# Kernel optimization log

Hardware: AMD Instinct MI355X
Metric: run time of the kernel (lower is better)

The kernel has to match this reference:

```python
import jax, jax.numpy as jnp
import numpy as np

B, S, D, HD, P = 4, 8192, 1024, 128, 32
EPS_LN = 1e-5

def setup_inputs() -> dict:
    key = jax.random.key(0)
    ks = jax.random.split(key, 12)
    x      = jax.random.normal(ks[0], (B, S, D), dtype=jnp.float32)
    W_proj = jax.random.normal(ks[1], (8, D, HD), dtype=jnp.float32) * 0.02
    freqs  = jax.random.normal(ks[2], (8, HD), dtype=jnp.float32) * 0.01
    W_pol  = jax.random.normal(ks[3], (8, HD, P), dtype=jnp.float32) * 0.05
    b_pol  = jnp.zeros((8, P), jnp.float32)
    W_imp1 = jax.random.normal(ks[4], (1, 16), dtype=jnp.float32) * 0.5
    b_imp1 = jnp.zeros((16,), jnp.float32)
    W_imp2 = jax.random.normal(ks[5], (16, 1), dtype=jnp.float32) * 0.5
    b_imp2 = jnp.zeros((1,), jnp.float32)
    W_out  = jax.random.normal(ks[6], (D, D), dtype=jnp.float32) * 0.02
    b_out  = jnp.zeros((D,), jnp.float32)
    gamma  = jnp.ones((D,), jnp.float32)
    beta   = jnp.zeros((D,), jnp.float32)
    return dict(x=x, W_proj=W_proj, freqs=freqs, W_pol=W_pol, b_pol=b_pol,
                W_imp1=W_imp1, b_imp1=b_imp1, W_imp2=W_imp2, b_imp2=b_imp2,
                W_out=W_out, b_out=b_out, gamma=gamma, beta=beta)

def reference(x, W_proj, freqs, W_pol, b_pol, W_imp1, b_imp1, W_imp2, b_imp2,
              W_out, b_out, gamma, beta):
    # heads[i] = (x @ W_proj[i]) * cos(pi * freqs[i])   -> (8, B, S, HD)
    heads = jnp.einsum('bsd,hde->hbse', x, W_proj) * jnp.cos(freqs * jnp.pi)[:, None, None, :]

    # --- GuaXiangDuiChong: impedance matrix (B, 8, 8) ---
    hm = heads.mean(axis=2)                                   # (8, B, HD)
    pv = jnp.tanh(jnp.einsum('hbd,hdp->bhp', hm, W_pol) + b_pol[None])  # (B, 8, P)
    pm = pv / jnp.maximum(jnp.linalg.norm(pv, axis=-1, keepdims=True), 1e-12)
    dp = jnp.einsum('bhp,bgp->bhg', pm, pm)                   # (B, 8, 8)
    z = jax.nn.gelu(dp[..., None] * W_imp1[0] + b_imp1, approximate=False)  # (B,8,8,16)
    imp = jax.nn.softplus(jnp.einsum('bhgk,ko->bhgo', z, W_imp2)[..., 0] + b_imp2[0])
    imp = imp * (1.0 - jnp.eye(8, dtype=imp.dtype))           # zero diagonal

    # --- head mixing. Causal masked-mean collapses to row scale (s+1)/S ---
    coeff = (0.1 / (1.0 + imp)) * (1.0 - jnp.eye(8, dtype=imp.dtype))  # (B,8,8), j!=i
    mix = jnp.einsum('big,gbsd->ibsd', coeff, heads)          # (8, B, S, HD)
    causal_scale = (jnp.arange(S, dtype=x.dtype) + 1.0) / S   # (S,)
    out_heads = heads + causal_scale[None, None, :, None] * mix

    merged = out_heads.transpose(1, 2, 0, 3).reshape(B, S, D)
    proj = jnp.einsum('bsd,de->bse', merged, W_out) + b_out   # dropout = identity (eval)
    y = proj + x
    mu = y.mean(axis=-1, keepdims=True)
    var = y.var(axis=-1, keepdims=True)
    y = (y - mu) * jax.lax.rsqrt(var + EPS_LN) * gamma + beta
    return y, imp
```

## Files before the change

kernel.cpp:

```cpp
#include <hip/hip_runtime.h>
#include <hip/hip_bf16.h>
#include <math.h>

typedef __bf16 bf16;
typedef __bf16 bf16x2 __attribute__((ext_vector_type(2)));
typedef __bf16 bf16x4 __attribute__((ext_vector_type(4)));
typedef __bf16 bf16x8 __attribute__((ext_vector_type(8)));
typedef float  f32x4  __attribute__((ext_vector_type(4)));

#define NB 4
#define SS 8192
#define DD 1024
#define MM 32768
#define KK 1024
#define NN 1024
#define PI_F 3.14159265358979323846f

__device__ __forceinline__ void gl2lds16(const bf16* g, bf16* l) {
    __builtin_amdgcn_global_load_lds(
        (const __attribute__((address_space(1))) void*)g,
        (__attribute__((address_space(3))) void*)l, 16, 0, 0);
}

__global__ __launch_bounds__(256) void prep_all(const float* __restrict__ x,
                                                bf16* __restrict__ xb,
                                                const float* __restrict__ W_proj,
                                                const float* __restrict__ freqs,
                                                const float* __restrict__ W_out,
                                                bf16* __restrict__ WbT1,
                                                bf16* __restrict__ WoT,
                                                float* __restrict__ hm) {
    int blk = blockIdx.x;
    if (blk < MM / 2) {
        size_t i = (size_t)blk * 2048 + threadIdx.x * 8;
        float4 v0 = *(const float4*)&x[i];
        float4 v1 = *(const float4*)&x[i + 4];
        bf16x8 o;
        o[0] = (bf16)v0.x; o[1] = (bf16)v0.y; o[2] = (bf16)v0.z; o[3] = (bf16)v0.w;
        o[4] = (bf16)v1.x; o[5] = (bf16)v1.y; o[6] = (bf16)v1.z; o[7] = (bf16)v1.w;
        *(bf16x8*)&xb[i] = o;
    } else {
        int idx = (blk - MM / 2) * 256 + threadIdx.x;
        int n = idx >> 10, k = idx & 1023;
        int h = n >> 7, d = n & 127;
        float c = cosf(PI_F * freqs[n]);
        WbT1[idx] = (bf16)(W_proj[(size_t)h * (DD * 128) + (size_t)k * 128 + d] * c);
        WoT[idx]  = (bf16)(W_out[(size_t)k * DD + n]);
        if (idx < NB * DD) hm[idx] = 0.0f;
    }
}


#define FENCE  asm volatile("" ::: "memory")
#define BARRIER do { FENCE; __builtin_amdgcn_s_barrier(); FENCE; } while (0)
#define PRIO1  __builtin_amdgcn_s_setprio(1)
#define PRIO0  __builtin_amdgcn_s_setprio(0)
#define VMC(N) asm volatile("s_waitcnt vmcnt(" #N ")" ::: "memory")
#define NOPS   ((void)0)

#define STG(g0, g1, uk, ldsBase)                                  \
    gl2lds16((g0) + (uk), &sm[(ldsBase) + w * 512]);              \
    gl2lds16((g1) + (uk), &sm[(ldsBase) + 4096 + w * 512]);

#define READ_A2(MQ, ab)                                                          \
    _Pragma("unroll") for (int m_ = 0; m_ < 4; ++m_) {                           \
        a[m_ * 2 + 0] = *(const bf16x8*)&sm[(ab) + aoff0 + ((MQ)*64 + m_*16)*64];\
        a[m_ * 2 + 1] = *(const bf16x8*)&sm[(ab) + aoff1 + ((MQ)*64 + m_*16)*64];\
    }
#define READ_B2(NQ, bfr, bb)                                                     \
    _Pragma("unroll") for (int n_ = 0; n_ < 2; ++n_) {                           \
        bfr[n_ * 2 + 0] = *(const bf16x8*)&sm[(bb) + boff0 + ((NQ)*32 + n_*16)*64];\
        bfr[n_ * 2 + 1] = *(const bf16x8*)&sm[(bb) + boff1 + ((NQ)*32 + n_*16)*64];\
    }

#define MFMA_Q(MQ, NQ, bfr)                                                    \
    _Pragma("unroll") for (int m_ = 0; m_ < 4; ++m_)                           \
    _Pragma("unroll") for (int n_ = 0; n_ < 2; ++n_)                           \
    _Pragma("unroll") for (int ks_ = 0; ks_ < 2; ++ks_)                        \
        acc[(MQ) * 4 + m_][(NQ) * 2 + n_] =                                    \
            __builtin_amdgcn_mfma_f32_16x16x32_bf16(                           \
                a[m_ * 2 + ks_], bfr[n_ * 2 + ks_],                            \
                acc[(MQ) * 4 + m_][(NQ) * 2 + n_], 0, 0, 0);

#define ITER(uk1, STGB2a, STGB2b, STGA2a, STGA2b, STGB3a, STGB3b, VM2, VM4)    \
  {                        \
    BARRIER;                                                                   \
    STG(gA00, gA01, (uk1), 16384); STG(gA10, gA11, (uk1), 24576);              \
    PRIO1; READ_A2(0, 0); READ_B2(0, blo, 32768); READ_B2(1, bhi, 32768);      \
    MFMA_Q(0, 0, blo); MFMA_Q(0, 1, bhi); PRIO0;                               \
                          \
    BARRIER;                                                                   \
    STGB2a; STGB2b; VM2;                                                       \
    PRIO1; READ_A2(1, 0); MFMA_Q(1, 1, bhi); MFMA_Q(1, 0, blo); PRIO0;         \
                         \
    BARRIER;                                                                   \
    STGA2a; STGA2b;                                                            \
    PRIO1; READ_A2(0, 16384); READ_B2(0, blo, 49152); READ_B2(1, bhi, 49152);  \
    MFMA_Q(0, 0, blo); MFMA_Q(0, 1, bhi); PRIO0;                               \
                          \
    BARRIER;                                                                   \
    STGB3a; STGB3b; VM4;                                                       \
    PRIO1; READ_A2(1, 16384); MFMA_Q(1, 1, bhi); MFMA_Q(1, 0, blo); PRIO0;     \
  }

template <int MODE>
__global__ __launch_bounds__(512, 2)
void gemm256(const bf16* __restrict__ A, int lda, const bf16* __restrict__ Bt,
             bf16* __restrict__ Cstr, const bf16* __restrict__ residb,
             const float* __restrict__ bias, float* __restrict__ hm) {
    __shared__ bf16 sm[65536];
    const int tid = threadIdx.x;
    const int lane = tid & 63, w = tid >> 6;
    const int wr = w >> 2, wc = w & 3;
    const int l15 = lane & 15, l4 = lane >> 4;

    int wg = blockIdx.x;
    int swz = (wg & 7) * 64 + (wg >> 3);
    const int mt = swz >> 2, ntile = swz & 3;
    const int row0 = mt * 256, col0 = ntile * 256;

    const int aoff0 = (wr * 128 + l15) * 64 + ((l4 ^ (l15 & 7)) << 3);
    const int aoff1 = aoff0 ^ 32;
    const int boff0 = (wc * 64 + l15) * 64 + ((l4 ^ (l15 & 7)) << 3);
    const int boff1 = boff0 ^ 32;

    const int srow = tid >> 3;
    const int scb  = (tid & 7) ^ (srow & 7);
    const bf16* gA00 = A + (size_t)(row0 + srow) * lda + scb * 8;
    const bf16* gA01 = gA00 + (size_t)64 * lda;
    const bf16* gA10 = gA00 + (size_t)128 * lda;
    const bf16* gA11 = gA00 + (size_t)192 * lda;
    const bf16* gB00 = Bt + (size_t)(col0 + srow) * 1024 + scb * 8;
    const bf16* gB01 = gB00 + 64 * 1024;
    const bf16* gB10 = gB00 + 128 * 1024;
    const bf16* gB11 = gB00 + 192 * 1024;

    f32x4 acc[8][4] = {};
    bf16x8 a[8], blo[4], bhi[4];

    STG(gA00, gA01, 0,  0);     STG(gA10, gA11, 0,  8192);
    STG(gB00, gB01, 0,  32768); STG(gB10, gB11, 0,  40960);
    STG(gB00, gB01, 64, 49152); STG(gB10, gB11, 64, 57344);
    VMC(4);

#pragma unroll 1
    for (int i = 0; i < 7; ++i) {
        const int uk1 = (2 * i + 1) * 64;
        const int uk2 = (2 * i + 2) * 64;
        const int uk3 = (2 * i + 3) * 64;
        ITER(uk1,
             STG(gB00, gB01, uk2, 32768), STG(gB10, gB11, uk2, 40960),
             STG(gA00, gA01, uk2, 0),     STG(gA10, gA11, uk2, 8192),
             STG(gB00, gB01, uk3, 49152), STG(gB10, gB11, uk3, 57344),
             VMC(4), VMC(4));
    }
    ITER(960, NOPS, NOPS, NOPS, NOPS, NOPS, NOPS, VMC(0), NOPS);

    if (MODE == 0) {
        const int batch = row0 >> 13;
#pragma unroll
        for (int mg = 0; mg < 8; ++mg) {
            int rbase = row0 + wr * 128 + (mg >> 2) * 64 + (mg & 3) * 16 + l4 * 4;
#pragma unroll
            for (int j = 0; j < 4; ++j) {
                size_t row = rbase + j;
#pragma unroll
                for (int ng = 0; ng < 4; ++ng) {
                    int col = col0 + wc * 64 + ng * 16 + l15;
                    Cstr[row * 2048 + col] = (bf16)acc[mg][ng][j];
                }
            }
        }
#pragma unroll
        for (int ng = 0; ng < 4; ++ng) {
            float s = 0;
#pragma unroll
            for (int mg = 0; mg < 8; ++mg)
#pragma unroll
                for (int j = 0; j < 4; ++j) s += acc[mg][ng][j];
            int col = col0 + wc * 64 + ng * 16 + l15;
            atomicAdd(&hm[batch * DD + col], s);
        }
    } else {
        float bi[4];
#pragma unroll
        for (int ng = 0; ng < 4; ++ng) bi[ng] = bias[col0 + wc * 64 + ng * 16 + l15];
#pragma unroll
        for (int mg = 0; mg < 8; ++mg) {
            int rbase = row0 + wr * 128 + (mg >> 2) * 64 + (mg & 3) * 16 + l4 * 4;
#pragma unroll
            for (int j = 0; j < 4; ++j) {
                size_t row = rbase + j;
#pragma unroll
                for (int ng = 0; ng < 4; ++ng) {
                    int col = col0 + wc * 64 + ng * 16 + l15;
                    Cstr[row * 2048 + col] =
                        (bf16)(acc[mg][ng][j] + bi[ng] + (float)residb[row * 1024 + col]);
                }
            }
        }
    }
}

__global__ __launch_bounds__(1024) void imp_k(const float* __restrict__ hm,
                                              const float* __restrict__ W_pol,
                                              const float* __restrict__ b_pol,
                                              const float* __restrict__ W_imp1,
                                              const float* __restrict__ b_imp1,
                                              const float* __restrict__ W_imp2,
                                              const float* __restrict__ b_imp2,
                                              float* __restrict__ imp_out,
                                              float* __restrict__ coeff) {
    __shared__ float pm_s[32][32];
    int tid = threadIdx.x;
    int bh = tid >> 5, p = tid & 31;
    int b = bh >> 3, h = bh & 7;
    float a = b_pol[h * 32 + p];
    for (int d = 0; d < 128; ++d)
        a += hm[b * DD + h * 128 + d] * (1.0f / SS) * W_pol[(h * 128 + d) * 32 + p];
    float pv = tanhf(a);
    pm_s[bh][p] = pv;
    __syncthreads();
    float ss = 0;
    for (int q = 0; q < 32; ++q) ss += pm_s[bh][q] * pm_s[bh][q];
    float pmv = pv / fmaxf(sqrtf(ss), 1e-12f);
    __syncthreads();
    pm_s[bh][p] = pmv;
    __syncthreads();
    if (tid < 256) {
        int b2 = tid >> 6, h2 = (tid >> 3) & 7, g = tid & 7;
        float dp = 0;
        for (int q = 0; q < 32; ++q) dp += pm_s[b2 * 8 + h2][q] * pm_s[b2 * 8 + g][q];
        float a2 = 0;
        for (int kk = 0; kk < 16; ++kk) {
            float zin = dp * W_imp1[kk] + b_imp1[kk];
            float zg = 0.5f * zin * (1.0f + erff(zin * 0.70710678118654752f));
            a2 += zg * W_imp2[kk];
        }
        float spin = a2 + b_imp2[0];
        float impv = (spin > 20.0f) ? spin : log1pf(expf(spin));
        if (h2 == g) impv = 0.0f;
        imp_out[tid] = impv;
        coeff[tid] = (h2 == g) ? 0.0f : 0.1f / (1.0f + impv);
    }
}

__global__ __launch_bounds__(256) void mix_k(const char* __restrict__ slots,
                                             const float* __restrict__ coeff,
                                             char* __restrict__ slots_w) {
    __shared__ float cf[64];
    int tid = threadIdx.x;
    size_t r0 = (size_t)blockIdx.x * 16;
    int b = (int)(r0 >> 13);
    if (tid < 64) cf[tid] = coeff[b * 64 + tid];
    __syncthreads();
    size_t r = r0 + (tid >> 4);
    int dd = tid & 15;
    int s = (int)(r & (SS - 1));
    float cs = (float)(s + 1) * (1.0f / SS);
    const bf16* hrow = (const bf16*)(slots + r * 4096);
    bf16* mrow = (bf16*)(slots_w + r * 4096 + 2048);
    float v[8][8];
#pragma unroll
    for (int g = 0; g < 8; ++g) {
        bf16x8 t8 = *(const bf16x8*)&hrow[g * 128 + dd * 8];
#pragma unroll
        for (int e = 0; e < 8; ++e) v[g][e] = (float)t8[e];
    }
#pragma unroll
    for (int h = 0; h < 8; ++h) {
        bf16x8 o;
#pragma unroll
        for (int e = 0; e < 8; ++e) {
            float acc = 0;
#pragma unroll
            for (int g = 0; g < 8; ++g) acc += cf[h * 8 + g] * v[g][e];
            o[e] = (bf16)(v[h][e] + cs * acc);
        }
        *(bf16x8*)&mrow[h * 128 + dd * 8] = o;
    }
}

__global__ __launch_bounds__(256) void ln_k(char* __restrict__ slots,
                                            const float* __restrict__ gamma,
                                            const float* __restrict__ beta) {
    size_t r = blockIdx.x;
    int tid = threadIdx.x;
    const bf16* zrow = (const bf16*)(slots + r * 4096);
    float* yrow = (float*)(slots + r * 4096);
    int e0 = tid * 4;
    bf16x4 zv = *(const bf16x4*)&zrow[e0];
    float vx = (float)zv[0], vy = (float)zv[1], vz = (float)zv[2], vw = (float)zv[3];
    float sum = vx + vy + vz + vw;
    float sq  = vx * vx + vy * vy + vz * vz + vw * vw;
    for (int off = 32; off > 0; off >>= 1) {
        sum += __shfl_down(sum, off);
        sq  += __shfl_down(sq, off);
    }
    __shared__ float red[8];
    int lane = tid & 63, wv = tid >> 6;
    if (lane == 0) { red[wv] = sum; red[4 + wv] = sq; }
    __syncthreads();
    float tot = red[0] + red[1] + red[2] + red[3];
    float tsq = red[4] + red[5] + red[6] + red[7];
    float mu  = tot * (1.0f / DD);
    float var = tsq * (1.0f / DD) - mu * mu;
    float rs  = rsqrtf(var + 1e-5f);
    float4 g4 = *(const float4*)&gamma[e0];
    float4 b4 = *(const float4*)&beta[e0];
    float4 o;
    o.x = (vx - mu) * rs * g4.x + b4.x;
    o.y = (vy - mu) * rs * g4.y + b4.y;
    o.z = (vz - mu) * rs * g4.z + b4.z;
    o.w = (vw - mu) * rs * g4.w + b4.w;
    *(float4*)&yrow[e0] = o;
}

extern "C" void kernel_launch(void* const* d_in, const int* in_sizes, int n_in,
                              void* d_out, int out_size, void* d_ws, size_t ws_size,
                              hipStream_t stream) {
    const float* x      = (const float*)d_in[0];
    const float* W_proj = (const float*)d_in[1];
    const float* freqs  = (const float*)d_in[2];
    const float* W_pol  = (const float*)d_in[3];
    const float* b_pol  = (const float*)d_in[4];
    const float* W_imp1 = (const float*)d_in[5];
    const float* b_imp1 = (const float*)d_in[6];
    const float* W_imp2 = (const float*)d_in[7];
    const float* b_imp2 = (const float*)d_in[8];
    const float* W_out  = (const float*)d_in[9];
    const float* b_out  = (const float*)d_in[10];
    const float* gamma  = (const float*)d_in[11];
    const float* beta   = (const float*)d_in[12];

    char* ws = (char*)d_ws;
    bf16* xb     = (bf16*)ws;
    bf16* WbT1   = (bf16*)(ws + ((size_t)64 << 20));
    bf16* WoT    = (bf16*)(ws + ((size_t)66 << 20));
    float* hm    = (float*)(ws + ((size_t)68 << 20));
    float* coeff = (float*)(ws + ((size_t)68 << 20) + 16384);

    char* slots = (char*)d_out;
    float* imp_out = (float*)d_out + (size_t)MM * DD;

    prep_all<<<MM / 2 + 4096, 256, 0, stream>>>(x, xb, W_proj, freqs, W_out,
                                                WbT1, WoT, hm);

    gemm256<0><<<512, 512, 0, stream>>>(xb, 1024, WbT1, (bf16*)slots,
                                        nullptr, nullptr, hm);

    imp_k<<<1, 1024, 0, stream>>>(hm, W_pol, b_pol, W_imp1, b_imp1, W_imp2, b_imp2,
                                  imp_out, coeff);

    mix_k<<<MM / 16, 256, 0, stream>>>(slots, coeff, slots);

    gemm256<1><<<512, 512, 0, stream>>>((const bf16*)slots + 1024, 2048, WoT,
                                        (bf16*)slots, xb, b_out, nullptr);

    ln_k<<<MM, 256, 0, stream>>>(slots, gamma, beta);
}
```

Before: 272.3 us.

## Split GEMM main loop into finer barrier phases, parallelize impedance, batch LayerNorm rows

```diff
diff --git a/kernel.cpp b/kernel.cpp
--- a/kernel.cpp
+++ b/kernel.cpp
@@ -50,7 +50,6 @@
     }
 }
 
-
 #define FENCE  asm volatile("" ::: "memory")
 #define BARRIER do { FENCE; __builtin_amdgcn_s_barrier(); FENCE; } while (0)
 #define PRIO1  __builtin_amdgcn_s_setprio(1)
@@ -82,25 +81,23 @@
                 a[m_ * 2 + ks_], bfr[n_ * 2 + ks_],                            \
                 acc[(MQ) * 4 + m_][(NQ) * 2 + n_], 0, 0, 0);
 
-#define ITER(uk1, STGB2a, STGB2b, STGA2a, STGA2b, STGB3a, STGB3b, VM2, VM4)    \
-  {                        \
-    BARRIER;                                                                   \
-    STG(gA00, gA01, (uk1), 16384); STG(gA10, gA11, (uk1), 24576);              \
-    PRIO1; READ_A2(0, 0); READ_B2(0, blo, 32768); READ_B2(1, bhi, 32768);      \
-    MFMA_Q(0, 0, blo); MFMA_Q(0, 1, bhi); PRIO0;                               \
-                          \
-    BARRIER;                                                                   \
-    STGB2a; STGB2b; VM2;                                                       \
-    PRIO1; READ_A2(1, 0); MFMA_Q(1, 1, bhi); MFMA_Q(1, 0, blo); PRIO0;         \
-                         \
-    BARRIER;                                                                   \
-    STGA2a; STGA2b;                                                            \
-    PRIO1; READ_A2(0, 16384); READ_B2(0, blo, 49152); READ_B2(1, bhi, 49152);  \
-    MFMA_Q(0, 0, blo); MFMA_Q(0, 1, bhi); PRIO0;                               \
-                          \
-    BARRIER;                                                                   \
-    STGB3a; STGB3b; VM4;                                                       \
-    PRIO1; READ_A2(1, 16384); MFMA_Q(1, 1, bhi); MFMA_Q(1, 0, blo); PRIO0;     \
+#define ITER(uk1, STG3, STG4, STG5, STG6, STG7, STG8, VM4, VM8)                \
+  { BARRIER; STG(gA00, gA01, (uk1), 16384);                                    \
+    PRIO1; READ_A2(0, 0); READ_B2(0, blo, 32768); MFMA_Q(0, 0, blo); PRIO0;    \
+    BARRIER; STG(gA10, gA11, (uk1), 24576);                                    \
+    PRIO1; READ_B2(1, bhi, 32768); MFMA_Q(0, 1, bhi); PRIO0;                   \
+    BARRIER; STG3;                                                             \
+    PRIO1; READ_A2(1, 0); MFMA_Q(1, 1, bhi); PRIO0;                            \
+    BARRIER; STG4; VM4;                                                        \
+    PRIO1; MFMA_Q(1, 0, blo); PRIO0;                                           \
+    BARRIER; STG5;                                                             \
+    PRIO1; READ_A2(0, 16384); READ_B2(0, blo, 49152); MFMA_Q(0, 0, blo); PRIO0;\
+    BARRIER; STG6;                                                             \
+    PRIO1; READ_B2(1, bhi, 49152); MFMA_Q(0, 1, bhi); PRIO0;                   \
+    BARRIER; STG7;                                                             \
+    PRIO1; READ_A2(1, 16384); MFMA_Q(1, 1, bhi); PRIO0;                        \
+    BARRIER; STG8; VM8;                                                        \
+    PRIO1; MFMA_Q(1, 0, blo); PRIO0;                                           \
   }
 
 template <int MODE>
@@ -140,8 +137,9 @@
 
     STG(gA00, gA01, 0,  0);     STG(gA10, gA11, 0,  8192);
     STG(gB00, gB01, 0,  32768); STG(gB10, gB11, 0,  40960);
+    STG(gA00, gA01, 64, 16384); STG(gA10, gA11, 64, 24576);
     STG(gB00, gB01, 64, 49152); STG(gB10, gB11, 64, 57344);
-    VMC(4);
+    VMC(0);
 
 #pragma unroll 1
     for (int i = 0; i < 7; ++i) {
@@ -202,47 +200,63 @@
     }
 }
 
-__global__ __launch_bounds__(1024) void imp_k(const float* __restrict__ hm,
+__global__ __launch_bounds__(256) void imp_pm(const float* __restrict__ hm,
                                               const float* __restrict__ W_pol,
                                               const float* __restrict__ b_pol,
-                                              const float* __restrict__ W_imp1,
-                                              const float* __restrict__ b_imp1,
-                                              const float* __restrict__ W_imp2,
-                                              const float* __restrict__ b_imp2,
-                                              float* __restrict__ imp_out,
-                                              float* __restrict__ coeff) {
-    __shared__ float pm_s[32][32];
+                                              float* __restrict__ pm) {
+    int bh = blockIdx.x;
+    int b = bh >> 3, h = bh & 7;
     int tid = threadIdx.x;
-    int bh = tid >> 5, p = tid & 31;
-    int b = bh >> 3, h = bh & 7;
-    float a = b_pol[h * 32 + p];
-    for (int d = 0; d < 128; ++d)
-        a += hm[b * DD + h * 128 + d] * (1.0f / SS) * W_pol[(h * 128 + d) * 32 + p];
-    float pv = tanhf(a);
-    pm_s[bh][p] = pv;
+    int p = tid & 31, dg = tid >> 5;
+    float partial = 0;
+#pragma unroll
+    for (int dd = 0; dd < 16; ++dd) {
+        int d = dg * 16 + dd;
+        partial += hm[b * DD + h * 128 + d] * (1.0f / SS)
+                 * W_pol[(h * 128 + d) * 32 + p];
+    }
+    __shared__ float red[8][32];
+    red[dg][p] = partial;
     __syncthreads();
-    float ss = 0;
-    for (int q = 0; q < 32; ++q) ss += pm_s[bh][q] * pm_s[bh][q];
-    float pmv = pv / fmaxf(sqrtf(ss), 1e-12f);
+    if (tid < 32) {
+        float a = b_pol[h * 32 + p];
+#pragma unroll
+        for (int g = 0; g < 8; ++g) a += red[g][p];
+        float pv = tanhf(a);
+        float ss = pv * pv;
+#pragma unroll
+        for (int off = 16; off > 0; off >>= 1) ss += __shfl_xor(ss, off);
+        pm[bh * 32 + p] = pv / fmaxf(sqrtf(ss), 1e-12f);
+    }
+}
+
+__global__ __launch_bounds__(256) void imp_mlp(const float* __restrict__ pm,
+                                               const float* __restrict__ W_imp1,
+                                               const float* __restrict__ b_imp1,
+                                               const float* __restrict__ W_imp2,
+                                               const float* __restrict__ b_imp2,
+                                               float* __restrict__ imp_out,
+                                               float* __restrict__ coeff) {
+    __shared__ float pms[32][32];
+    int tid = threadIdx.x;
+    for (int i = tid; i < 1024; i += 256) pms[i >> 5][i & 31] = pm[i];
     __syncthreads();
-    pm_s[bh][p] = pmv;
-    __syncthreads();
-    if (tid < 256) {
-        int b2 = tid >> 6, h2 = (tid >> 3) & 7, g = tid & 7;
-        float dp = 0;
-        for (int q = 0; q < 32; ++q) dp += pm_s[b2 * 8 + h2][q] * pm_s[b2 * 8 + g][q];
-        float a2 = 0;
-        for (int kk = 0; kk < 16; ++kk) {
-            float zin = dp * W_imp1[kk] + b_imp1[kk];
-            float zg = 0.5f * zin * (1.0f + erff(zin * 0.70710678118654752f));
-            a2 += zg * W_imp2[kk];
-        }
-        float spin = a2 + b_imp2[0];
-        float impv = (spin > 20.0f) ? spin : log1pf(expf(spin));
-        if (h2 == g) impv = 0.0f;
-        imp_out[tid] = impv;
-        coeff[tid] = (h2 == g) ? 0.0f : 0.1f / (1.0f + impv);
-    }
+    int b2 = tid >> 6, h2 = (tid >> 3) & 7, g = tid & 7;
+    float dp = 0;
+#pragma unroll
+    for (int q = 0; q < 32; ++q) dp += pms[b2 * 8 + h2][q] * pms[b2 * 8 + g][q];
+    float a2 = 0;
+#pragma unroll
+    for (int kk = 0; kk < 16; ++kk) {
+        float zin = dp * W_imp1[kk] + b_imp1[kk];
+        float zg = 0.5f * zin * (1.0f + erff(zin * 0.70710678118654752f));
+        a2 += zg * W_imp2[kk];
+    }
+    float spin = a2 + b_imp2[0];
+    float impv = (spin > 20.0f) ? spin : log1pf(expf(spin));
+    if (h2 == g) impv = 0.0f;
+    imp_out[tid] = impv;
+    coeff[tid] = (h2 == g) ? 0.0f : 0.1f / (1.0f + impv);
 }
 
 __global__ __launch_bounds__(256) void mix_k(const char* __restrict__ slots,
@@ -284,36 +298,51 @@
 __global__ __launch_bounds__(256) void ln_k(char* __restrict__ slots,
                                             const float* __restrict__ gamma,
                                             const float* __restrict__ beta) {
-    size_t r = blockIdx.x;
     int tid = threadIdx.x;
+    size_t r = (size_t)blockIdx.x * 2 + (tid >> 7);
+    int t = tid & 127;
     const bf16* zrow = (const bf16*)(slots + r * 4096);
     float* yrow = (float*)(slots + r * 4096);
-    int e0 = tid * 4;
-    bf16x4 zv = *(const bf16x4*)&zrow[e0];
-    float vx = (float)zv[0], vy = (float)zv[1], vz = (float)zv[2], vw = (float)zv[3];
-    float sum = vx + vy + vz + vw;
-    float sq  = vx * vx + vy * vy + vz * vz + vw * vw;
+    int e0 = t * 8;
+    bf16x8 zv = *(const bf16x8*)&zrow[e0];
+    float v[8];
+    float sum = 0, sq = 0;
+#pragma unroll
+    for (int e = 0; e < 8; ++e) {
+        v[e] = (float)zv[e];
+        sum += v[e];
+        sq  += v[e] * v[e];
+    }
+#pragma unroll
     for (int off = 32; off > 0; off >>= 1) {
         sum += __shfl_down(sum, off);
         sq  += __shfl_down(sq, off);
     }
-    __shared__ float red[8];
+    __shared__ float red[4][2];
     int lane = tid & 63, wv = tid >> 6;
-    if (lane == 0) { red[wv] = sum; red[4 + wv] = sq; }
+    if (lane == 0) { red[wv][0] = sum; red[wv][1] = sq; }
     __syncthreads();
-    float tot = red[0] + red[1] + red[2] + red[3];
-    float tsq = red[4] + red[5] + red[6] + red[7];
+    int rw = (tid >> 7) * 2;
+    float tot = red[rw][0] + red[rw + 1][0];
+    float tsq = red[rw][1] + red[rw + 1][1];
     float mu  = tot * (1.0f / DD);
     float var = tsq * (1.0f / DD) - mu * mu;
     float rs  = rsqrtf(var + 1e-5f);
-    float4 g4 = *(const float4*)&gamma[e0];
-    float4 b4 = *(const float4*)&beta[e0];
-    float4 o;
-    o.x = (vx - mu) * rs * g4.x + b4.x;
-    o.y = (vy - mu) * rs * g4.y + b4.y;
-    o.z = (vz - mu) * rs * g4.z + b4.z;
-    o.w = (vw - mu) * rs * g4.w + b4.w;
-    *(float4*)&yrow[e0] = o;
+    float4 g0 = *(const float4*)&gamma[e0];
+    float4 g1 = *(const float4*)&gamma[e0 + 4];
+    float4 b0 = *(const float4*)&beta[e0];
+    float4 b1 = *(const float4*)&beta[e0 + 4];
+    float4 o0, o1;
+    o0.x = (v[0] - mu) * rs * g0.x + b0.x;
+    o0.y = (v[1] - mu) * rs * g0.y + b0.y;
+    o0.z = (v[2] - mu) * rs * g0.z + b0.z;
+    o0.w = (v[3] - mu) * rs * g0.w + b0.w;
+    o1.x = (v[4] - mu) * rs * g1.x + b1.x;
+    o1.y = (v[5] - mu) * rs * g1.y + b1.y;
+    o1.z = (v[6] - mu) * rs * g1.z + b1.z;
+    o1.w = (v[7] - mu) * rs * g1.w + b1.w;
+    *(float4*)&yrow[e0] = o0;
+    *(float4*)&yrow[e0 + 4] = o1;
 }
 
 extern "C" void kernel_launch(void* const* d_in, const int* in_sizes, int n_in,
@@ -339,6 +368,7 @@
     bf16* WoT    = (bf16*)(ws + ((size_t)66 << 20));
     float* hm    = (float*)(ws + ((size_t)68 << 20));
     float* coeff = (float*)(ws + ((size_t)68 << 20) + 16384);
+    float* pm    = (float*)(ws + ((size_t)68 << 20) + 20480);
 
     char* slots = (char*)d_out;
     float* imp_out = (float*)d_out + (size_t)MM * DD;
@@ -349,13 +379,14 @@
     gemm256<0><<<512, 512, 0, stream>>>(xb, 1024, WbT1, (bf16*)slots,
                                         nullptr, nullptr, hm);
 
-    imp_k<<<1, 1024, 0, stream>>>(hm, W_pol, b_pol, W_imp1, b_imp1, W_imp2, b_imp2,
-                                  imp_out, coeff);
+    imp_pm<<<32, 256, 0, stream>>>(hm, W_pol, b_pol, pm);
+    imp_mlp<<<1, 256, 0, stream>>>(pm, W_imp1, b_imp1, W_imp2, b_imp2,
+                                   imp_out, coeff);
 
     mix_k<<<MM / 16, 256, 0, stream>>>(slots, coeff, slots);
 
     gemm256<1><<<512, 512, 0, stream>>>((const bf16*)slots + 1024, 2048, WoT,
                                         (bf16*)slots, xb, b_out, nullptr);
 
-    ln_k<<<MM, 256, 0, stream>>>(slots, gamma, beta);
-}
+    ln_k<<<MM / 2, 256, 0, stream>>>(slots, gamma, beta);
+}
```

Result: faster. 264.4 us, median of 2 (-2.9%).
